# Kernel optimization log

Measured on AMD Instinct MI355X. Metric: run time of the kernel, lower is better.

## Reference

```python
import jax, jax.numpy as jnp
import numpy as np

B, T, D, H, E = 4, 2048, 1024, 4096, 8


def setup_inputs() -> dict:
    key = jax.random.key(0)
    ks = jax.random.split(key, 7)
    x = jax.random.normal(ks[0], (B, T, D), dtype=jnp.float32)
    # Gate: Linear(D, E)
    Wg = jax.random.normal(ks[1], (D, E), dtype=jnp.float32) / np.sqrt(D)
    bg = jax.random.normal(ks[2], (E,), dtype=jnp.float32) * 0.01
    # Experts: E x [Linear(D,H), ReLU, Linear(H,D)] (dropout inactive at eval)
    W1 = jax.random.normal(ks[3], (E, D, H), dtype=jnp.float32) / np.sqrt(D)
    b1 = jax.random.normal(ks[4], (E, H), dtype=jnp.float32) * 0.01
    W2 = jax.random.normal(ks[5], (E, H, D), dtype=jnp.float32) / np.sqrt(H)
    b2 = jax.random.normal(ks[6], (E, D), dtype=jnp.float32) * 0.01
    return {"x": x, "Wg": Wg, "bg": bg, "W1": W1, "b1": b1, "W2": W2, "b2": b2}


def reference(x, Wg, bg, W1, b1, W2, b2):
    # Gate + hard top-1 routing
    gate_scores = x @ Wg + bg                      # [B,T,E]
    top1 = jnp.argmax(gate_scores, axis=-1)        # [B,T]
    onehot = jax.nn.one_hot(top1, Wg.shape[-1], dtype=x.dtype)  # [B,T,E]
    # Dense: every expert MLP over all tokens (matches original's masked
    # formulation: x*mask == x on selected tokens, output re-masked).
    h = jax.nn.relu(jnp.einsum('btd,edh->beth', x, W1) + b1[None, :, None, :])
    y = jnp.einsum('beth,ehd->betd', h, W2) + b2[None, :, None, :]
    # Masked combine: keep only the token's chosen expert output
    out = jnp.einsum('betd,bte->btd', y, onehot)
    return out
```

## Files before the change

### kernel.cpp

```cpp
#include <hip/hip_runtime.h>
#include <hip/hip_bf16.h>
#include <stdint.h>

#define NTOK 8192
#define DDIM 1024
#define HDIM 4096
#define NEXP 8
#define MAXWL1 48
#define MAXWL2 72

typedef __attribute__((ext_vector_type(4))) float f32x4;
typedef __attribute__((ext_vector_type(8))) short s16x8;
typedef __attribute__((ext_vector_type(8))) unsigned short u16x8;

__device__ __forceinline__ unsigned short f2bf(float f) {
  union { float f; unsigned int u; } v; v.f = f;
  unsigned int u = v.u;
  u += 0x7FFFu + ((u >> 16) & 1u);
  return (unsigned short)(u >> 16);
}

typedef __attribute__((address_space(3))) unsigned char lds_u8;
typedef const __attribute__((address_space(1))) unsigned char glb_u8;

__device__ __forceinline__ void load_lds16(const void* g, void* l) {
  __builtin_amdgcn_global_load_lds((glb_u8*)g, (lds_u8*)l, 16, 0, 0);
}

__global__ __launch_bounds__(256) void gate_kernel(
    const float* __restrict__ x, const float* __restrict__ Wg,
    const float* __restrict__ bg, int* __restrict__ counts,
    int* __restrict__ lists) {
  const int lane = threadIdx.x & 63;
  const int tok = blockIdx.x * 4 + (threadIdx.x >> 6);
  const float* xr = x + (size_t)tok * DDIM;
  double acc[NEXP];
#pragma unroll
  for (int e = 0; e < NEXP; ++e) acc[e] = 0.0;
#pragma unroll 4
  for (int it = 0; it < DDIM / 64; ++it) {
    const int d = it * 64 + lane;
    const float xv = xr[d];
    const f32x4 w0 = *(const f32x4*)(Wg + (size_t)d * NEXP);
    const f32x4 w1 = *(const f32x4*)(Wg + (size_t)d * NEXP + 4);
#pragma unroll
    for (int j = 0; j < 4; ++j) {
      acc[j]     += (double)xv * (double)w0[j];
      acc[4 + j] += (double)xv * (double)w1[j];
    }
  }
#pragma unroll
  for (int e = 0; e < NEXP; ++e) {
    double v = acc[e];
#pragma unroll
    for (int off = 32; off > 0; off >>= 1) v += __shfl_xor(v, off, 64);
    acc[e] = v;
  }
  if (lane == 0) {
    int best = 0;
    double bv = acc[0] + (double)bg[0];
#pragma unroll
    for (int e = 1; e < NEXP; ++e) {
      const double v = acc[e] + (double)bg[e];
      if (v > bv) { bv = v; best = e; }
    }
    const int pos = atomicAdd(&counts[best], 1);
    lists[best * NTOK + pos] = tok;
  }
}

__global__ void offs_kernel(const int* __restrict__ counts, int* __restrict__ offs,
                            int* __restrict__ wl1, int* __restrict__ wl2) {
  int s = 0;
#pragma unroll
  for (int e = 0; e < NEXP; ++e) { offs[e] = s; s += counts[e]; }
  offs[NEXP] = s;
  int n1 = 0, n2 = 0;
  for (int e = 0; e < NEXP; ++e) {
    const int nb1 = (counts[e] + 255) >> 8;
    for (int b = 0; b < nb1; ++b) wl1[n1++] = (e << 20) | b;
    const int nb2 = (counts[e] + 127) >> 7;
    for (int b = 0; b < nb2; ++b) wl2[n2++] = (e << 20) | b;
  }
  offs[NEXP + 1] = n1;
  offs[NEXP + 2] = n2;
}

__global__ __launch_bounds__(256) void gather_conv_kernel(
    const float* __restrict__ x, const int* __restrict__ offs,
    const int* __restrict__ lists, int* __restrict__ stok,
    unsigned short* __restrict__ xbs) {
  const int p = blockIdx.x * 4 + (threadIdx.x >> 6);
  const int lane = threadIdx.x & 63;
  int e = 0;
#pragma unroll
  for (int k = 1; k < NEXP; ++k) e += (p >= offs[k]) ? 1 : 0;
  const int tok = lists[e * NTOK + (p - offs[e])];
  if (lane == 0) stok[p] = tok;
  const float* src = x + (size_t)tok * DDIM + lane * 16;
  unsigned short* dst = xbs + (size_t)p * DDIM + lane * 16;
#pragma unroll
  for (int q = 0; q < 2; ++q) {
    const f32x4 a = *(const f32x4*)(src + q * 8);
    const f32x4 b = *(const f32x4*)(src + q * 8 + 4);
    u16x8 o;
#pragma unroll
    for (int j = 0; j < 4; ++j) { o[j] = f2bf(a[j]); o[4 + j] = f2bf(b[j]); }
    *(u16x8*)(dst + q * 8) = o;
  }
}

__global__ __launch_bounds__(256) void transpose_conv_kernel(
    const float* __restrict__ in, unsigned short* __restrict__ out,
    int R, int C) {
  __shared__ unsigned short T[64][66];
  const int e = blockIdx.z;
  const float* ine = in + (size_t)e * R * C;
  unsigned short* oute = out + (size_t)e * C * R;
  const int c0 = blockIdx.x * 64, r0 = blockIdx.y * 64;
  const int t = threadIdx.x;
  const int tr = t >> 4, tc4 = (t & 15) * 4;
#pragma unroll
  for (int p = 0; p < 4; ++p) {
    const int r = tr + p * 16;
    const f32x4 v = *(const f32x4*)(ine + (size_t)(r0 + r) * C + c0 + tc4);
#pragma unroll
    for (int j = 0; j < 4; ++j) T[r][tc4 + j] = f2bf(v[j]);
  }
  __syncthreads();
  const int cc = t >> 3, rr8 = (t & 7) * 8;
#pragma unroll
  for (int p = 0; p < 2; ++p) {
    const int c = cc + p * 32;
    u16x8 o;
#pragma unroll
    for (int j = 0; j < 8; ++j) o[j] = T[rr8 + j][c];
    *(u16x8*)(oute + (size_t)(c0 + c) * R + r0 + rr8) = o;
  }
}

template <int BM, int BN, int WM, int WN, int K, int N, int MAXWLT,
          bool COLFAST, bool FUSE1>
__global__ __launch_bounds__(512, 4) void ffn_kernel(
    const unsigned short* __restrict__ A, const unsigned short* __restrict__ Bt,
    const float* __restrict__ bias, const int* __restrict__ counts,
    const int* __restrict__ offs, const int* __restrict__ wl,
    const int* __restrict__ stok, unsigned short* __restrict__ outb,
    float* __restrict__ outf, int nwl_idx) {
  constexpr int MF = BM / (WM * 16);
  constexpr int NF = BN / (WN * 16);
  constexpr int ISS_A = BM / 128;
  constexpr int ISS_B = BN / 128;
  constexpr int NT = K / 32;
  constexpr int NCB = N / BN;
  constexpr int NWG = NCB * MAXWLT;
  static_assert((NWG & 7) == 0 && (NT & 1) == 0 && NT >= 4, "");
  static_assert(WM * WN == 8, "8 waves");

  const int d = blockIdx.x;
  const int logical = (d & 7) * (NWG / 8) + (d >> 3);
  int cb, wli;
  if constexpr (COLFAST) { cb = logical % NCB; wli = logical / NCB; }
  else                   { cb = logical / MAXWLT; wli = logical % MAXWLT; }
  if (wli >= offs[nwl_idx]) return;
  const int col0 = cb * BN;
  const int wle = wl[wli];
  const int e = wle >> 20;
  const int bx = wle & 0xFFFFF;
  const int cnt = counts[e];
  const int row0 = offs[e] + bx * BM;

  __shared__ __align__(16) unsigned short As0[BM * 32], Bs0[BN * 32];
  __shared__ __align__(16) unsigned short As1[BM * 32], Bs1[BN * 32];

  const int tid = threadIdx.x;
  const int lane = tid & 63;
  const int w = tid >> 6;
  const int wm = w / WN;
  const int wn = w % WN;
  const int fr = lane & 15;
  const int fj = lane >> 4;

  const int swsrc = ((tid & 3) ^ ((tid >> 3) & 3)) * 8;
  const int rb = tid >> 2;
  const unsigned short* srcA[ISS_A];
#pragma unroll
  for (int i = 0; i < ISS_A; ++i) {
    int gr = row0 + i * 128 + rb;
    if (gr > NTOK - 1) gr = NTOK - 1;
    srcA[i] = A + (size_t)gr * K + swsrc;
  }
  const unsigned short* Bte = Bt + (size_t)e * N * K;
  const unsigned short* srcB[ISS_B];
#pragma unroll
  for (int i = 0; i < ISS_B; ++i)
    srcB[i] = Bte + (size_t)(col0 + i * 128 + rb) * K + swsrc;

  const int js = (fj ^ ((fr >> 1) & 3)) * 8;

  f32x4 acc[MF][NF];
#pragma unroll
  for (int m = 0; m < MF; ++m)
#pragma unroll
    for (int n = 0; n < NF; ++n) acc[m][n] = f32x4{0.f, 0.f, 0.f, 0.f};

  auto stage = [&](unsigned short* dA, unsigned short* dB, int kel) {
#pragma unroll
    for (int i = 0; i < ISS_A; ++i)
      load_lds16(srcA[i] + kel, dA + i * 4096 + tid * 8);
#pragma unroll
    for (int i = 0; i < ISS_B; ++i)
      load_lds16(srcB[i] + kel, dB + i * 4096 + tid * 8);
  };

  auto phase = [&](const unsigned short* pA, const unsigned short* pB,
                   unsigned short* nA, unsigned short* nB, int knext,
                   bool do_stage) {
    asm volatile("s_waitcnt vmcnt(0)" ::: "memory");
    __builtin_amdgcn_s_barrier();
    asm volatile("" ::: "memory");
    s16x8 af[MF], bf[NF];
#pragma unroll
    for (int m = 0; m < MF; ++m)
      af[m] = *(const s16x8*)(pA + (wm * MF * 16 + m * 16 + fr) * 32 + js);
#pragma unroll
    for (int n = 0; n < NF; ++n)
      bf[n] = *(const s16x8*)(pB + (wn * NF * 16 + n * 16 + fr) * 32 + js);
    if (do_stage) stage(nA, nB, knext);
    __builtin_amdgcn_s_setprio(1);
#pragma unroll
    for (int m = 0; m < MF; ++m)
#pragma unroll
      for (int n = 0; n < NF; ++n)
        acc[m][n] = __builtin_amdgcn_mfma_f32_16x16x32_bf16(af[m], bf[n],
                                                            acc[m][n], 0, 0, 0);
    __builtin_amdgcn_s_setprio(0);
  };

  stage(As0, Bs0, 0);
#pragma unroll 1
  for (int t = 0; t < NT - 2; t += 2) {
    phase(As0, Bs0, As1, Bs1, (t + 1) * 32, true);
    phase(As1, Bs1, As0, Bs0, (t + 2) * 32, true);
  }
  phase(As0, Bs0, As1, Bs1, (NT - 1) * 32, true);
  phase(As1, Bs1, nullptr, nullptr, 0, false);

#pragma unroll
  for (int n = 0; n < NF; ++n) {
    const int col = col0 + wn * NF * 16 + n * 16 + fr;
    const float bv = bias[e * N + col];
#pragma unroll
    for (int m = 0; m < MF; ++m) {
#pragma unroll
      for (int j = 0; j < 4; ++j) {
        const int rl = wm * MF * 16 + m * 16 + fj * 4 + j;
        if (bx * BM + rl < cnt) {
          if constexpr (FUSE1) {
            outb[(size_t)(row0 + rl) * N + col] = f2bf(fmaxf(acc[m][n][j] + bv, 0.f));
          } else {
            outf[(size_t)stok[row0 + rl] * N + col] = acc[m][n][j] + bv;
          }
        }
      }
    }
  }
}

extern "C" void kernel_launch(void* const* d_in, const int* in_sizes, int n_in,
                              void* d_out, int out_size, void* d_ws, size_t ws_size,
                              hipStream_t stream) {
  (void)in_sizes; (void)n_in; (void)out_size;
  const float* x  = (const float*)d_in[0];
  const float* Wg = (const float*)d_in[1];
  const float* bg = (const float*)d_in[2];
  const float* W1 = (const float*)d_in[3];
  const float* b1 = (const float*)d_in[4];
  const float* W2 = (const float*)d_in[5];
  const float* b2 = (const float*)d_in[6];
  float* out = (float*)d_out;

  char* ws = (char*)d_ws;
  const size_t OFF_CNT = 0;
  const size_t OFF_OFF = 128;
  const size_t OFF_WL1 = 256;
  const size_t OFF_WL2 = 256 + MAXWL1 * 4;
  const size_t OFF_LST = 1024;
  const size_t OFF_STK = OFF_LST + (size_t)NEXP * NTOK * 4;
  const size_t OFF_XBS = OFF_STK + (size_t)NTOK * 4;
  const size_t OFF_HS  = OFF_XBS + (size_t)NTOK * DDIM * 2;
  const size_t OFF_WT  = OFF_HS + (size_t)NTOK * HDIM * 2;
  const size_t NEED    = OFF_WT + (size_t)NEXP * DDIM * HDIM * 2;
  if (ws_size < NEED) return;

  int* counts = (int*)(ws + OFF_CNT);
  int* offs   = (int*)(ws + OFF_OFF);
  int* wl1    = (int*)(ws + OFF_WL1);
  int* wl2    = (int*)(ws + OFF_WL2);
  int* lists  = (int*)(ws + OFF_LST);
  int* stok   = (int*)(ws + OFF_STK);
  unsigned short* xbs = (unsigned short*)(ws + OFF_XBS);
  unsigned short* Hs  = (unsigned short*)(ws + OFF_HS);
  unsigned short* Wt  = (unsigned short*)(ws + OFF_WT);

  hipMemsetAsync(counts, 0, 128, stream);
  gate_kernel<<<NTOK / 4, 256, 0, stream>>>(x, Wg, bg, counts, lists);
  offs_kernel<<<1, 1, 0, stream>>>(counts, offs, wl1, wl2);
  gather_conv_kernel<<<NTOK / 4, 256, 0, stream>>>(x, offs, lists, stok, xbs);

  transpose_conv_kernel<<<dim3(HDIM / 64, DDIM / 64, NEXP), 256, 0, stream>>>(
      W1, Wt, DDIM, HDIM);
  ffn_kernel<256, 128, 4, 2, DDIM, HDIM, MAXWL1, false, true>
      <<<dim3((HDIM / 128) * MAXWL1), 512, 0, stream>>>(
          xbs, Wt, b1, counts, offs, wl1, stok, Hs, nullptr, NEXP + 1);
  transpose_conv_kernel<<<dim3(DDIM / 64, HDIM / 64, NEXP), 256, 0, stream>>>(
      W2, Wt, HDIM, DDIM);
  ffn_kernel<128, 256, 2, 4, HDIM, DDIM, MAXWL2, true, false>
      <<<dim3((DDIM / 256) * MAXWL2), 512, 0, stream>>>(
          Hs, Wt, b2, counts, offs, wl2, stok, nullptr, out, NEXP + 2);
}
```

Baseline: 453.0 us.

## Triple-buffer FFN GEMM LDS pipeline with partial vmcnt waits; vectorize transpose

The FFN GEMM main loop moves from double to triple LDS buffering. It prefetches two k-tiles ahead and waits with vmcnt(S) instead of vmcnt(0), so global-to-LDS loads stay in flight across an extra MFMA phase. The transpose/convert kernel is also rewritten to transpose 4x4 blocks in registers, write ushort4 to padded LDS, and emit two 16-byte stores per thread. The third LDS buffer raises shared-memory use per block, which may reduce how many blocks fit per CU.

```diff
diff --git a/kernel.cpp b/kernel.cpp
--- a/kernel.cpp
+++ b/kernel.cpp
@@ -25,6 +25,14 @@
 
 __device__ __forceinline__ void load_lds16(const void* g, void* l) {
   __builtin_amdgcn_global_load_lds((glb_u8*)g, (lds_u8*)l, 16, 0, 0);
+}
+
+template <int VM> __device__ __forceinline__ void wait_vm() {
+  if constexpr (VM == 6)      asm volatile("s_waitcnt vmcnt(6)" ::: "memory");
+  else if constexpr (VM == 4) asm volatile("s_waitcnt vmcnt(4)" ::: "memory");
+  else if constexpr (VM == 3) asm volatile("s_waitcnt vmcnt(3)" ::: "memory");
+  else if constexpr (VM == 2) asm volatile("s_waitcnt vmcnt(2)" ::: "memory");
+  else                        asm volatile("s_waitcnt vmcnt(0)" ::: "memory");
 }
 
 __global__ __launch_bounds__(256) void gate_kernel(
@@ -113,30 +121,32 @@
 __global__ __launch_bounds__(256) void transpose_conv_kernel(
     const float* __restrict__ in, unsigned short* __restrict__ out,
     int R, int C) {
-  __shared__ unsigned short T[64][66];
+  __shared__ __align__(16) unsigned short T[64][68];
   const int e = blockIdx.z;
   const float* ine = in + (size_t)e * R * C;
   unsigned short* oute = out + (size_t)e * C * R;
   const int c0 = blockIdx.x * 64, r0 = blockIdx.y * 64;
   const int t = threadIdx.x;
-  const int tr = t >> 4, tc4 = (t & 15) * 4;
-#pragma unroll
-  for (int p = 0; p < 4; ++p) {
-    const int r = tr + p * 16;
-    const f32x4 v = *(const f32x4*)(ine + (size_t)(r0 + r) * C + c0 + tc4);
-#pragma unroll
-    for (int j = 0; j < 4; ++j) T[r][tc4 + j] = f2bf(v[j]);
+  const int rb = (t >> 4) * 4;
+  const int cb = (t & 15) * 4;
+  f32x4 v[4];
+#pragma unroll
+  for (int j = 0; j < 4; ++j)
+    v[j] = *(const f32x4*)(ine + (size_t)(r0 + rb + j) * C + c0 + cb);
+#pragma unroll
+  for (int i = 0; i < 4; ++i) {
+    ushort4 o;
+    o.x = f2bf(v[0][i]); o.y = f2bf(v[1][i]);
+    o.z = f2bf(v[2][i]); o.w = f2bf(v[3][i]);
+    *(ushort4*)&T[cb + i][rb] = o;
   }
   __syncthreads();
-  const int cc = t >> 3, rr8 = (t & 7) * 8;
-#pragma unroll
-  for (int p = 0; p < 2; ++p) {
-    const int c = cc + p * 32;
-    u16x8 o;
-#pragma unroll
-    for (int j = 0; j < 8; ++j) o[j] = T[rr8 + j][c];
-    *(u16x8*)(oute + (size_t)(c0 + c) * R + r0 + rr8) = o;
-  }
+  const int c = t >> 2, q = (t & 3) * 16;
+  u16x8 o0, o1;
+#pragma unroll
+  for (int j = 0; j < 8; ++j) { o0[j] = T[c][q + j]; o1[j] = T[c][q + 8 + j]; }
+  *(u16x8*)(oute + (size_t)(c0 + c) * R + r0 + q) = o0;
+  *(u16x8*)(oute + (size_t)(c0 + c) * R + r0 + q + 8) = o1;
 }
 
 template <int BM, int BN, int WM, int WN, int K, int N, int MAXWLT,
@@ -151,10 +161,11 @@
   constexpr int NF = BN / (WN * 16);
   constexpr int ISS_A = BM / 128;
   constexpr int ISS_B = BN / 128;
+  constexpr int S = ISS_A + ISS_B;
   constexpr int NT = K / 32;
   constexpr int NCB = N / BN;
   constexpr int NWG = NCB * MAXWLT;
-  static_assert((NWG & 7) == 0 && (NT & 1) == 0 && NT >= 4, "");
+  static_assert((NWG & 7) == 0 && (NT % 3) == 2 && NT >= 5, "");
   static_assert(WM * WN == 8, "8 waves");
 
   const int d = blockIdx.x;
@@ -172,6 +183,7 @@
 
   __shared__ __align__(16) unsigned short As0[BM * 32], Bs0[BN * 32];
   __shared__ __align__(16) unsigned short As1[BM * 32], Bs1[BN * 32];
+  __shared__ __align__(16) unsigned short As2[BM * 32], Bs2[BN * 32];
 
   const int tid = threadIdx.x;
   const int lane = tid & 63;
@@ -213,10 +225,9 @@
       load_lds16(srcB[i] + kel, dB + i * 4096 + tid * 8);
   };
 
-  auto phase = [&](const unsigned short* pA, const unsigned short* pB,
-                   unsigned short* nA, unsigned short* nB, int knext,
-                   bool do_stage) {
-    asm volatile("s_waitcnt vmcnt(0)" ::: "memory");
+  auto body = [&](const unsigned short* pA, const unsigned short* pB,
+                  unsigned short* nA, unsigned short* nB, int knext,
+                  bool do_stage) {
     __builtin_amdgcn_s_barrier();
     asm volatile("" ::: "memory");
     s16x8 af[MF], bf[NF];
@@ -238,13 +249,16 @@
   };
 
   stage(As0, Bs0, 0);
+  stage(As1, Bs1, 32);
+
 #pragma unroll 1
-  for (int t = 0; t < NT - 2; t += 2) {
-    phase(As0, Bs0, As1, Bs1, (t + 1) * 32, true);
-    phase(As1, Bs1, As0, Bs0, (t + 2) * 32, true);
-  }
-  phase(As0, Bs0, As1, Bs1, (NT - 1) * 32, true);
-  phase(As1, Bs1, nullptr, nullptr, 0, false);
+  for (int t = 0; t < NT - 2; t += 3) {
+    wait_vm<S>(); body(As0, Bs0, As2, Bs2, (t + 2) * 32, true);
+    wait_vm<S>(); body(As1, Bs1, As0, Bs0, (t + 3) * 32, true);
+    wait_vm<S>(); body(As2, Bs2, As1, Bs1, (t + 4) * 32, true);
+  }
+  wait_vm<S>(); body(As0, Bs0, nullptr, nullptr, 0, false);
+  wait_vm<0>(); body(As1, Bs1, nullptr, nullptr, 0, false);
 
 #pragma unroll
   for (int n = 0; n < NF; ++n) {
```

After: 457.6 us. No clear change (+1.0%).

## Fuse fp32 weight transpose and bf16 conversion into the FFN GEMM B-load

Applied to the files above, without the earlier changes.

Removes the two separate transpose_conv kernels that converted W1/W2 to transposed bf16 in workspace. The GEMM now reads fp32 weights directly into registers, converts them to bf16 and writes them swizzled into LDS. The pipeline is restructured with a triple-buffered A and double-buffered B, and the register-staged B loads are issued one stage ahead. This saves a full pass over the 256 MB of fp32 weights plus the bf16 write and re-read. In exchange, weights are now re-read as fp32 by every row block, which raises per-tile global traffic and register pressure, and it adds an lgkmcnt wait.

```diff
diff --git a/kernel.cpp b/kernel.cpp
--- a/kernel.cpp
+++ b/kernel.cpp
@@ -110,39 +110,10 @@
   }
 }
 
-__global__ __launch_bounds__(256) void transpose_conv_kernel(
-    const float* __restrict__ in, unsigned short* __restrict__ out,
-    int R, int C) {
-  __shared__ unsigned short T[64][66];
-  const int e = blockIdx.z;
-  const float* ine = in + (size_t)e * R * C;
-  unsigned short* oute = out + (size_t)e * C * R;
-  const int c0 = blockIdx.x * 64, r0 = blockIdx.y * 64;
-  const int t = threadIdx.x;
-  const int tr = t >> 4, tc4 = (t & 15) * 4;
-#pragma unroll
-  for (int p = 0; p < 4; ++p) {
-    const int r = tr + p * 16;
-    const f32x4 v = *(const f32x4*)(ine + (size_t)(r0 + r) * C + c0 + tc4);
-#pragma unroll
-    for (int j = 0; j < 4; ++j) T[r][tc4 + j] = f2bf(v[j]);
-  }
-  __syncthreads();
-  const int cc = t >> 3, rr8 = (t & 7) * 8;
-#pragma unroll
-  for (int p = 0; p < 2; ++p) {
-    const int c = cc + p * 32;
-    u16x8 o;
-#pragma unroll
-    for (int j = 0; j < 8; ++j) o[j] = T[rr8 + j][c];
-    *(u16x8*)(oute + (size_t)(c0 + c) * R + r0 + rr8) = o;
-  }
-}
-
 template <int BM, int BN, int WM, int WN, int K, int N, int MAXWLT,
           bool COLFAST, bool FUSE1>
 __global__ __launch_bounds__(512, 4) void ffn_kernel(
-    const unsigned short* __restrict__ A, const unsigned short* __restrict__ Bt,
+    const unsigned short* __restrict__ A, const float* __restrict__ Wf,
     const float* __restrict__ bias, const int* __restrict__ counts,
     const int* __restrict__ offs, const int* __restrict__ wl,
     const int* __restrict__ stok, unsigned short* __restrict__ outb,
@@ -150,11 +121,11 @@
   constexpr int MF = BM / (WM * 16);
   constexpr int NF = BN / (WN * 16);
   constexpr int ISS_A = BM / 128;
-  constexpr int ISS_B = BN / 128;
+  constexpr int NRUN = BN / 128;
   constexpr int NT = K / 32;
   constexpr int NCB = N / BN;
   constexpr int NWG = NCB * MAXWLT;
-  static_assert((NWG & 7) == 0 && (NT & 1) == 0 && NT >= 4, "");
+  static_assert((NWG & 7) == 0 && (NT % 6) == 2 && NT >= 8, "");
   static_assert(WM * WN == 8, "8 waves");
 
   const int d = blockIdx.x;
@@ -170,8 +141,8 @@
   const int cnt = counts[e];
   const int row0 = offs[e] + bx * BM;
 
-  __shared__ __align__(16) unsigned short As0[BM * 32], Bs0[BN * 32];
-  __shared__ __align__(16) unsigned short As1[BM * 32], Bs1[BN * 32];
+  __shared__ __align__(16) unsigned short A0[BM * 32], A1[BM * 32], A2[BM * 32];
+  __shared__ __align__(16) unsigned short B0[BN * 32], B1[BN * 32];
 
   const int tid = threadIdx.x;
   const int lane = tid & 63;
@@ -182,41 +153,57 @@
   const int fj = lane >> 4;
 
   const int swsrc = ((tid & 3) ^ ((tid >> 3) & 3)) * 8;
-  const int rb = tid >> 2;
+  const int rbA = tid >> 2;
   const unsigned short* srcA[ISS_A];
 #pragma unroll
   for (int i = 0; i < ISS_A; ++i) {
-    int gr = row0 + i * 128 + rb;
+    int gr = row0 + i * 128 + rbA;
     if (gr > NTOK - 1) gr = NTOK - 1;
     srcA[i] = A + (size_t)gr * K + swsrc;
   }
-  const unsigned short* Bte = Bt + (size_t)e * N * K;
-  const unsigned short* srcB[ISS_B];
-#pragma unroll
-  for (int i = 0; i < ISS_B; ++i)
-    srcB[i] = Bte + (size_t)(col0 + i * 128 + rb) * K + swsrc;
-
-  const int js = (fj ^ ((fr >> 1) & 3)) * 8;
-
-  f32x4 acc[MF][NF];
-#pragma unroll
-  for (int m = 0; m < MF; ++m)
-#pragma unroll
-    for (int n = 0; n < NF; ++n) acc[m][n] = f32x4{0.f, 0.f, 0.f, 0.f};
-
-  auto stage = [&](unsigned short* dA, unsigned short* dB, int kel) {
+  auto stageA = [&](unsigned short* dA, int kel) {
 #pragma unroll
     for (int i = 0; i < ISS_A; ++i)
       load_lds16(srcA[i] + kel, dA + i * 4096 + tid * 8);
-#pragma unroll
-    for (int i = 0; i < ISS_B; ++i)
-      load_lds16(srcB[i] + kel, dB + i * 4096 + tid * 8);
   };
 
-  auto phase = [&](const unsigned short* pA, const unsigned short* pB,
-                   unsigned short* nA, unsigned short* nB, int knext,
-                   bool do_stage) {
+  const int cl = tid & 127;
+  const int q  = tid >> 7;
+  const float* Wfe = Wf + (size_t)e * K * N;
+  float bregs[NRUN * 8];
+  auto loadB = [&](int kel) {
+#pragma unroll
+    for (int i = 0; i < NRUN; ++i) {
+      const float* bp = Wfe + (size_t)(kel + 8 * q) * N + col0 + 128 * i + cl;
+#pragma unroll
+      for (int j = 0; j < 8; ++j) bregs[i * 8 + j] = bp[(size_t)j * N];
+    }
+  };
+  auto writeB = [&](unsigned short* dB) {
+#pragma unroll
+    for (int i = 0; i < NRUN; ++i) {
+      u16x8 o;
+#pragma unroll
+      for (int j = 0; j < 8; ++j) o[j] = f2bf(bregs[i * 8 + j]);
+      const int row = 128 * i + cl;
+      const int slot = q ^ ((row >> 1) & 3);
+      *(u16x8*)(dB + row * 32 + slot * 8) = o;
+    }
+  };
+
+  const int js = (fj ^ ((fr >> 1) & 3)) * 8;
+
+  f32x4 acc[MF][NF];
+#pragma unroll
+  for (int m = 0; m < MF; ++m)
+#pragma unroll
+    for (int n = 0; n < NF; ++n) acc[m][n] = f32x4{0.f, 0.f, 0.f, 0.f};
+
+  auto body = [&](const unsigned short* pA, const unsigned short* pB,
+                  unsigned short* nA, int kissue, unsigned short* wB,
+                  bool dow, bool doi) {
     asm volatile("s_waitcnt vmcnt(0)" ::: "memory");
+    asm volatile("s_waitcnt lgkmcnt(0)" ::: "memory");
     __builtin_amdgcn_s_barrier();
     asm volatile("" ::: "memory");
     s16x8 af[MF], bf[NF];
@@ -226,7 +213,8 @@
 #pragma unroll
     for (int n = 0; n < NF; ++n)
       bf[n] = *(const s16x8*)(pB + (wn * NF * 16 + n * 16 + fr) * 32 + js);
-    if (do_stage) stage(nA, nB, knext);
+    if (dow) writeB(wB);
+    if (doi) { stageA(nA, kissue); loadB(kissue); }
     __builtin_amdgcn_s_setprio(1);
 #pragma unroll
     for (int m = 0; m < MF; ++m)
@@ -237,14 +225,22 @@
     __builtin_amdgcn_s_setprio(0);
   };
 
-  stage(As0, Bs0, 0);
+  stageA(A0, 0); loadB(0);
+  asm volatile("s_waitcnt vmcnt(0)" ::: "memory");
+  writeB(B0);
+  stageA(A1, 32); loadB(32);
+
 #pragma unroll 1
-  for (int t = 0; t < NT - 2; t += 2) {
-    phase(As0, Bs0, As1, Bs1, (t + 1) * 32, true);
-    phase(As1, Bs1, As0, Bs0, (t + 2) * 32, true);
-  }
-  phase(As0, Bs0, As1, Bs1, (NT - 1) * 32, true);
-  phase(As1, Bs1, nullptr, nullptr, 0, false);
+  for (int t = 0; t < NT - 2; t += 6) {
+    body(A0, B0, A2, (t + 2) * 32, B1, true, true);
+    body(A1, B1, A0, (t + 3) * 32, B0, true, true);
+    body(A2, B0, A1, (t + 4) * 32, B1, true, true);
+    body(A0, B1, A2, (t + 5) * 32, B0, true, true);
+    body(A1, B0, A0, (t + 6) * 32, B1, true, true);
+    body(A2, B1, A1, (t + 7) * 32, B0, true, true);
+  }
+  body(A0, B0, nullptr, 0, B1, true, false);
+  body(A1, B1, nullptr, 0, nullptr, false, false);
 
 #pragma unroll
   for (int n = 0; n < NF; ++n) {
@@ -289,8 +285,7 @@
   const size_t OFF_STK = OFF_LST + (size_t)NEXP * NTOK * 4;
   const size_t OFF_XBS = OFF_STK + (size_t)NTOK * 4;
   const size_t OFF_HS  = OFF_XBS + (size_t)NTOK * DDIM * 2;
-  const size_t OFF_WT  = OFF_HS + (size_t)NTOK * HDIM * 2;
-  const size_t NEED    = OFF_WT + (size_t)NEXP * DDIM * HDIM * 2;
+  const size_t NEED    = OFF_HS + (size_t)NTOK * HDIM * 2;
   if (ws_size < NEED) return;
 
   int* counts = (int*)(ws + OFF_CNT);
@@ -301,21 +296,16 @@
   int* stok   = (int*)(ws + OFF_STK);
   unsigned short* xbs = (unsigned short*)(ws + OFF_XBS);
   unsigned short* Hs  = (unsigned short*)(ws + OFF_HS);
-  unsigned short* Wt  = (unsigned short*)(ws + OFF_WT);
 
   hipMemsetAsync(counts, 0, 128, stream);
   gate_kernel<<<NTOK / 4, 256, 0, stream>>>(x, Wg, bg, counts, lists);
   offs_kernel<<<1, 1, 0, stream>>>(counts, offs, wl1, wl2);
   gather_conv_kernel<<<NTOK / 4, 256, 0, stream>>>(x, offs, lists, stok, xbs);
 
-  transpose_conv_kernel<<<dim3(HDIM / 64, DDIM / 64, NEXP), 256, 0, stream>>>(
-      W1, Wt, DDIM, HDIM);
   ffn_kernel<256, 128, 4, 2, DDIM, HDIM, MAXWL1, false, true>
       <<<dim3((HDIM / 128) * MAXWL1), 512, 0, stream>>>(
-          xbs, Wt, b1, counts, offs, wl1, stok, Hs, nullptr, NEXP + 1);
-  transpose_conv_kernel<<<dim3(DDIM / 64, HDIM / 64, NEXP), 256, 0, stream>>>(
-      W2, Wt, HDIM, DDIM);
+          xbs, W1, b1, counts, offs, wl1, stok, Hs, nullptr, NEXP + 1);
   ffn_kernel<128, 256, 2, 4, HDIM, DDIM, MAXWL2, true, false>
       <<<dim3((DDIM / 256) * MAXWL2), 512, 0, stream>>>(
-          Hs, Wt, b2, counts, offs, wl2, stok, nullptr, out, NEXP + 2);
-}
+          Hs, W2, b2, counts, offs, wl2, stok, nullptr, out, NEXP + 2);
+}
```

After: 1.036 ms. 129% more time.
